# Performance work log

Measured on AMD Instinct MI355X. Metric: run time of the kernel, lower is better.

Reference implementation:

```python
import jax, jax.numpy as jnp
import numpy as np

B, RES_IN, STRIDE, RES_OUT = 8, 64, 2, 32
C_IN, C_OUT = 256, 512
H, KD, RATIO = 8, 16, 4
VD = RATIO * KD                      # 64
KV_DIM = (RATIO + 1) * KD * H        # 640
Q_DIM = KD * H                       # 128
PROJ_IN = RATIO * KD * H             # 512
SEQ = RES_IN * RES_IN                # 4096
QLEN = RES_OUT * RES_OUT             # 1024
EPS = 1e-3                           # keras BatchNormalization default epsilon


def _bn(x, gamma, beta, mean, var):
    # inference-mode batch norm over the channel axis
    return (x - mean) * (gamma * jax.lax.rsqrt(var + EPS)) + beta


def _hard_swish(x):
    return x * jnp.clip(x + 3.0, 0.0, 6.0) * (1.0 / 6.0)


def setup_inputs() -> dict:
    key = jax.random.key(0)
    ks = jax.random.split(key, 16)
    def lin(k, fan_in, fan_out):
        return jax.random.normal(k, (fan_in, fan_out), jnp.float32) / np.sqrt(fan_in)
    def bn_params(k, c):
        k1, k2, k3 = jax.random.split(k, 3)
        gamma = 1.0 + 0.1 * jax.random.normal(k1, (c,), jnp.float32)
        beta = 0.1 * jax.random.normal(k2, (c,), jnp.float32)
        mean = 0.1 * jax.random.normal(k3, (c,), jnp.float32)
        var = jax.random.uniform(jax.random.fold_in(k, 7), (c,), jnp.float32, 0.5, 1.5)
        return gamma, beta, mean, var
    x = jax.random.normal(ks[0], (B, SEQ, C_IN), jnp.float32)
    Wkv = lin(ks[1], C_IN, KV_DIM); bkv = jnp.zeros((KV_DIM,), jnp.float32)
    g_kv, b_kv, m_kv, v_kv = bn_params(ks[2], KV_DIM)
    Wq = lin(ks[3], C_IN, Q_DIM); bq = jnp.zeros((Q_DIM,), jnp.float32)
    g_q, b_q, m_q, v_q = bn_params(ks[4], Q_DIM)
    Wp = lin(ks[5], PROJ_IN, C_OUT); bp = jnp.zeros((C_OUT,), jnp.float32)
    g_p, b_p, m_p, v_p = bn_params(ks[6], C_OUT)
    return {"x": x, "Wkv": Wkv, "bkv": bkv, "g_kv": g_kv, "b_kv": b_kv, "m_kv": m_kv, "v_kv": v_kv,
            "Wq": Wq, "bq": bq, "g_q": g_q, "b_q": b_q, "m_q": m_q, "v_q": v_q,
            "Wp": Wp, "bp": bp, "g_p": g_p, "b_p": b_p, "m_p": m_p, "v_p": v_p}


def reference(x, Wkv, bkv, g_kv, b_kv, m_kv, v_kv,
              Wq, bq, g_q, b_q, m_q, v_q,
              Wp, bp, g_p, b_p, m_p, v_p):
    scale = KD ** (-0.5)
    # keys/values: Dense + BN -> [B, SEQ, H, KD+VD]
    kv = _bn(x @ Wkv + bkv, g_kv, b_kv, m_kv, v_kv)
    kv = kv.reshape(B, SEQ, H, KD + VD)
    k = jnp.transpose(kv[..., :KD], (0, 2, 1, 3))          # [B, H, SEQ, KD]
    v = jnp.transpose(kv[..., KD:], (0, 2, 1, 3))          # [B, H, SEQ, VD]
    # strided query subsample: [B, SEQ, C] -> [B, QLEN, C]
    xq = x.reshape(B, RES_IN, RES_IN, C_IN)[:, ::STRIDE, ::STRIDE].reshape(B, QLEN, C_IN)
    q = _bn(xq @ Wq + bq, g_q, b_q, m_q, v_q)
    q = jnp.transpose(q.reshape(B, QLEN, H, KD), (0, 2, 1, 3))  # [B, H, QLEN, KD]
    attn = jnp.einsum('bhqd,bhkd->bhqk', q, k) * scale
    attn = jax.nn.softmax(attn, axis=-1)                   # [B, H, QLEN, SEQ]
    av = jnp.einsum('bhqk,bhkd->bhqd', attn, v)            # [B, H, QLEN, VD]
    # faithful to TF: transpose (0,1,3,2) then reshape to (B, -1, PROJ_IN)
    out = jnp.transpose(av, (0, 1, 3, 2)).reshape(B, -1, PROJ_IN)
    out = _bn(_hard_swish(out) @ Wp + bp, g_p, b_p, m_p, v_p)
    return out
```

## Files before the change

### kernel.cpp

```cpp
#include <hip/hip_runtime.h>

typedef __bf16 bf16_t;
typedef __bf16 bf16x4 __attribute__((ext_vector_type(4)));
typedef __bf16 bf16x8 __attribute__((ext_vector_type(8)));
typedef short s16x4 __attribute__((ext_vector_type(4)));
typedef float f32x4 __attribute__((ext_vector_type(4)));

#define BN_EPS 1e-3f

#define GLOAD_LDS16(g, l) \
  __builtin_amdgcn_global_load_lds((const __attribute__((address_space(1))) void*)(g), \
                                   (__attribute__((address_space(3))) void*)(l), 16, 0, 0)

__global__ __launch_bounds__(256) void cvt_f32_bf16(
    const float* __restrict__ in, bf16_t* __restrict__ out, long n)
{
  long i = ((long)blockIdx.x * 256 + threadIdx.x) * 8;
  if (i + 8 > n) return;
  f32x4 a = *(const f32x4*)(in + i);
  f32x4 b = *(const f32x4*)(in + i + 4);
  bf16x8 o;
  o[0] = (bf16_t)a[0]; o[1] = (bf16_t)a[1]; o[2] = (bf16_t)a[2]; o[3] = (bf16_t)a[3];
  o[4] = (bf16_t)b[0]; o[5] = (bf16_t)b[1]; o[6] = (bf16_t)b[2]; o[7] = (bf16_t)b[3];
  *(bf16x8*)(out + i) = o;
}

__global__ __launch_bounds__(256) void transpose_f32_bf16(
    const float* __restrict__ in, bf16_t* __restrict__ out, int R, int C)
{
  __shared__ bf16_t t[32][33];
  int bx = blockIdx.x * 32, by = blockIdx.y * 32;
  int tx = threadIdx.x, ty = threadIdx.y;
#pragma unroll
  for (int i = 0; i < 32; i += 8)
    t[ty + i][tx] = (bf16_t)in[(long)(by + ty + i) * C + (bx + tx)];
  __syncthreads();
#pragma unroll
  for (int i = 0; i < 32; i += 8)
    out[(long)(bx + ty + i) * R + (by + tx)] = t[tx][ty + i];
}

__global__ __launch_bounds__(256) void wkv_split_transpose(
    const float* __restrict__ in, bf16_t* __restrict__ outK, bf16_t* __restrict__ outV)
{
  __shared__ bf16_t t[32][33];
  int bx = blockIdx.x * 32, by = blockIdx.y * 32;
  int tx = threadIdx.x, ty = threadIdx.y;
#pragma unroll
  for (int i = 0; i < 32; i += 8)
    t[ty + i][tx] = (bf16_t)in[(long)(by + ty + i) * 640 + (bx + tx)];
  __syncthreads();
#pragma unroll
  for (int i = 0; i < 32; i += 8) {
    int c = bx + ty + i;
    int h = c / 80, r80 = c - h * 80;
    bf16_t v = t[tx][ty + i];
    if (r80 < 16)
      outK[(long)(h * 16 + r80) * 256 + (by + tx)] = v;
    else
      outV[(long)(h * 64 + (r80 - 16)) * 256 + (by + tx)] = v;
  }
}

__global__ __launch_bounds__(512, 1) void qkv_fused(
    const bf16_t* __restrict__ xb, const bf16_t* __restrict__ Wf,
    const float* __restrict__ bkv, const float* __restrict__ g_kv,
    const float* __restrict__ b_kv, const float* __restrict__ m_kv,
    const float* __restrict__ v_kv,
    const float* __restrict__ bq, const float* __restrict__ g_q,
    const float* __restrict__ b_q, const float* __restrict__ m_q,
    const float* __restrict__ v_q,
    bf16_t* __restrict__ Kbuf, bf16_t* __restrict__ Vtb, bf16_t* __restrict__ Qbuf)
{
  __shared__ __align__(16) char Xs[65536];
  __shared__ __align__(16) char Ws[65536];

  const int tid = threadIdx.x;
  const int lane = tid & 63, w = tid >> 6;
  const int quad = lane >> 4, l15 = lane & 15;
  const int wm = w >> 2, wn = w & 3;

  const int id = blockIdx.x;
  const int xcd = id & 7, slot = id >> 3;
  const int sd6 = slot / 6;
  const int mt = xcd * 32 + sd6;
  const int nt = slot - sd6 * 6;
  const int blockM = mt * 128, blockN = nt * 128;

  {
    const int r_lo = w * 2 + (lane >> 5);
    const int soff = ((lane & 31) ^ (r_lo & 7)) << 4;
#pragma unroll
    for (int rnd = 0; rnd < 8; rnd++) {
      const int row = rnd * 16 + r_lo;
      GLOAD_LDS16((const char*)xb + (long)(blockM + row) * 512 + soff,
                  &Xs[rnd * 8192 + w * 1024]);
      GLOAD_LDS16((const char*)Wf + (long)(blockN + row) * 512 + soff,
                  &Ws[rnd * 8192 + w * 1024]);
    }
  }
  __syncthreads();

  const int sw = l15 & 7;
  f32x4 acc[4][2] = {};
#pragma unroll
  for (int ks = 0; ks < 8; ks++) {
    const int u = ks * 4 + quad;
    const int su = (u ^ sw) << 4;
    bf16x8 af[4];
#pragma unroll
    for (int mi = 0; mi < 4; mi++)
      af[mi] = *(const bf16x8*)(&Xs[(wm * 64 + mi * 16 + l15) * 512 + su]);
    bf16x8 bf_[2];
#pragma unroll
    for (int ni = 0; ni < 2; ni++)
      bf_[ni] = *(const bf16x8*)(&Ws[(wn * 32 + ni * 16 + l15) * 512 + su]);
#pragma unroll
    for (int mi = 0; mi < 4; mi++)
#pragma unroll
      for (int ni = 0; ni < 2; ni++)
        acc[mi][ni] = __builtin_amdgcn_mfma_f32_16x16x32_bf16(af[mi], bf_[ni], acc[mi][ni], 0, 0, 0);
  }

#pragma unroll
  for (int ni = 0; ni < 2; ni++) {
    const int nfbase = blockN + wn * 32 + ni * 16;
    const int col = nfbase + l15;
    float s, t, bia;
    if (nfbase < 128) {
      int cp = (col >> 4) * 80 + (col & 15);
      s = g_kv[cp] / sqrtf(v_kv[cp] + BN_EPS);
      t = b_kv[cp] - m_kv[cp] * s;
      bia = bkv[cp];
      int h = col >> 4, d = col & 15;
#pragma unroll
      for (int mi = 0; mi < 4; mi++)
#pragma unroll
        for (int r = 0; r < 4; r++) {
          int grow = blockM + wm * 64 + mi * 16 + quad * 4 + r;
          int b = grow >> 12, seq = grow & 4095;
          float y = (acc[mi][ni][r] + bia) * s + t;
          Kbuf[((long)((b * 8 + h) * 4096 + seq)) * 16 + d] = (bf16_t)y;
        }
    } else if (nfbase < 640) {
      int ch = col - 128;
      int cp = (ch >> 6) * 80 + 16 + (ch & 63);
      s = g_kv[cp] / sqrtf(v_kv[cp] + BN_EPS);
      t = b_kv[cp] - m_kv[cp] * s;
      bia = bkv[cp];
      int h2 = ch >> 6, dv = ch & 63;
#pragma unroll
      for (int mi = 0; mi < 4; mi++)
#pragma unroll
        for (int r = 0; r < 4; r++) {
          int grow = blockM + wm * 64 + mi * 16 + quad * 4 + r;
          int b = grow >> 12, seq = grow & 4095;
          int kb = seq >> 5, s32 = seq & 31;
          int qd = (s32 & 15) >> 2, j = (s32 >> 4) * 4 + (s32 & 3);
          float y = (acc[mi][ni][r] + bia) * s + t;
          Vtb[(((long)(b * 8 + h2)) << 18) + (kb << 11) + (qd << 9) + (dv << 3) + j] = (bf16_t)y;
        }
    } else {
      int qc = col - 640;
      s = g_q[qc] / sqrtf(v_q[qc] + BN_EPS);
      t = b_q[qc] - m_q[qc] * s;
      bia = bq[qc];
      int h = qc >> 4, d = qc & 15;
#pragma unroll
      for (int mi = 0; mi < 4; mi++) {
        if ((((blockM + wm * 64 + mi * 16) >> 6) & 1) != 0) continue;
#pragma unroll
        for (int r = 0; r < 4; r += 2) {
          int grow = blockM + wm * 64 + mi * 16 + quad * 4 + r;
          int b = grow >> 12, seq = grow & 4095;
          int qp = ((seq >> 7) << 5) + ((seq & 63) >> 1);
          float y = (acc[mi][ni][r] + bia) * s + t;
          Qbuf[((long)((b * 8 + h) * 1024 + qp)) * 16 + d] = (bf16_t)(y * 0.36067376f);
        }
      }
    }
  }
}

__global__ __launch_bounds__(512, 1) void proj_fused(
    const bf16_t* __restrict__ A, const bf16_t* __restrict__ Wt,
    const float* __restrict__ bias, const float* __restrict__ gamma,
    const float* __restrict__ beta, const float* __restrict__ mean,
    const float* __restrict__ var, float* __restrict__ outf)
{
  __shared__ __align__(16) char Xs[65536];
  __shared__ __align__(16) char Wl[65536];

  const int tid = threadIdx.x;
  const int lane = tid & 63, w = tid >> 6;
  const int quad = lane >> 4, l15 = lane & 15;
  const int wm = w >> 2, wn = w & 3;

  const int id = blockIdx.x;
  const int xcd = id & 7, slot = id >> 3;
  const int mt = xcd * 8 + (slot >> 2);
  const int nt = slot & 3;
  const int blockM = mt * 128, blockN = nt * 128;

  const int r_lo = w * 2 + (lane >> 5);
  const int soff = ((lane & 31) ^ (r_lo & 7)) << 4;
  const int sw = l15 & 7;
  f32x4 acc[4][2] = {};

#pragma unroll
  for (int kc = 0; kc < 2; kc++) {
    if (kc) __syncthreads();
#pragma unroll
    for (int rnd = 0; rnd < 8; rnd++) {
      const int row = rnd * 16 + r_lo;
      GLOAD_LDS16((const char*)A  + (long)(blockM + row) * 1024 + kc * 512 + soff,
                  &Xs[rnd * 8192 + w * 1024]);
      GLOAD_LDS16((const char*)Wt + (long)(blockN + row) * 1024 + kc * 512 + soff,
                  &Wl[rnd * 8192 + w * 1024]);
    }
    __syncthreads();

#pragma unroll
    for (int ks = 0; ks < 8; ks++) {
      const int u = ks * 4 + quad;
      const int su = (u ^ sw) << 4;
      bf16x8 af[4];
#pragma unroll
      for (int mi = 0; mi < 4; mi++)
        af[mi] = *(const bf16x8*)(&Xs[(wm * 64 + mi * 16 + l15) * 512 + su]);
      bf16x8 bw[2];
#pragma unroll
      for (int ni = 0; ni < 2; ni++)
        bw[ni] = *(const bf16x8*)(&Wl[(wn * 32 + ni * 16 + l15) * 512 + su]);
#pragma unroll
      for (int mi = 0; mi < 4; mi++)
#pragma unroll
        for (int ni = 0; ni < 2; ni++)
          acc[mi][ni] = __builtin_amdgcn_mfma_f32_16x16x32_bf16(af[mi], bw[ni], acc[mi][ni], 0, 0, 0);
    }
  }

#pragma unroll
  for (int ni = 0; ni < 2; ni++) {
    int col = blockN + wn * 32 + ni * 16 + l15;
    float s = gamma[col] / sqrtf(var[col] + BN_EPS);
    float t = beta[col] - mean[col] * s;
    float bia = bias[col];
#pragma unroll
    for (int mi = 0; mi < 4; mi++)
#pragma unroll
      for (int r = 0; r < 4; r++) {
        int grow = blockM + wm * 64 + mi * 16 + quad * 4 + r;
        float y = (acc[mi][ni][r] + bia) * s + t;
        outf[(long)grow * 512 + col] = y;
      }
  }
}

__global__ __launch_bounds__(256, 4) void attn_kernel(
    const bf16_t* __restrict__ Q, const bf16_t* __restrict__ K,
    const bf16_t* __restrict__ Vt, bf16_t* __restrict__ outp)
{
  const int tid = threadIdx.x;
  const int lane = tid & 63, w = tid >> 6;
  const int quad = lane >> 4, l15 = lane & 15;
  const int bh = blockIdx.x & 63, qb = blockIdx.x >> 6;
  const int b = bh >> 3, h = bh & 7;
  const bf16_t* Qp = Q + (long)bh * 1024 * 16;
  const char* Kg = (const char*)(K + (long)bh * 4096 * 16);
  const char* Vg = (const char*)(Vt + ((long)bh << 18));

  __shared__ __align__(16) char Kl[4][2048];
  __shared__ __align__(16) char Vl[4][8192];

  const int q0 = qb * 64 + w * 16;
  bf16x8 qB8;
  {
    bf16x8 qv = *(const bf16x8*)(Qp + (long)(q0 + l15) * 16 + (quad & 1) * 8);
    bf16x8 zq = {};
    qB8 = (quad < 2) ? qv : zq;
  }

  f32x4 O[4] = {};
  f32x4 lpacc = {};
  const f32x4 zf = {0.f, 0.f, 0.f, 0.f};

  bf16x8 ones8;
#pragma unroll
  for (int i = 0; i < 8; i++) ones8[i] = (bf16_t)1.f;

  const char* vsrc = Vg + (long)lane * 16;
  const char* ksrc = Kg + (long)lane * 32 + (w - 2) * 16;

  auto stage = [&](int t, int buf) {
    if (w < 2) {
#pragma unroll
      for (int c = 0; c < 2; c++)
        GLOAD_LDS16(vsrc + (long)t * 8192 + (w * 2 + c) * 1024, &Vl[buf][(w * 2 + c) * 1024]);
    } else {
#pragma unroll
      for (int c = 0; c < 2; c++)
        GLOAD_LDS16(vsrc + (long)t * 8192 + ((w - 2) * 2 + 4 + c) * 1024,
                    &Vl[buf][((w - 2) * 2 + 4 + c) * 1024]);
      GLOAD_LDS16(ksrc + (long)t * 2048, &Kl[buf][(w - 2) * 1024]);
    }
  };

  const int krow_off = (quad & 1) * 1024;

  auto compute = [&](int buf) {
#pragma unroll
    for (int kh = 0; kh < 2; kh++) {
      bf16x8 k0 = *(const bf16x8*)(&Kl[buf][krow_off + (kh * 32 + l15) * 16]);
      bf16x8 k1 = *(const bf16x8*)(&Kl[buf][krow_off + (kh * 32 + 16 + l15) * 16]);
      f32x4 S0 = __builtin_amdgcn_mfma_f32_16x16x32_bf16(k0, qB8, zf, 0, 0, 0);
      f32x4 S1 = __builtin_amdgcn_mfma_f32_16x16x32_bf16(k1, qB8, zf, 0, 0, 0);
      bf16x8 pb;
      pb[0] = (bf16_t)__builtin_amdgcn_exp2f(S0[0]);
      pb[1] = (bf16_t)__builtin_amdgcn_exp2f(S0[1]);
      pb[2] = (bf16_t)__builtin_amdgcn_exp2f(S0[2]);
      pb[3] = (bf16_t)__builtin_amdgcn_exp2f(S0[3]);
      pb[4] = (bf16_t)__builtin_amdgcn_exp2f(S1[0]);
      pb[5] = (bf16_t)__builtin_amdgcn_exp2f(S1[1]);
      pb[6] = (bf16_t)__builtin_amdgcn_exp2f(S1[2]);
      pb[7] = (bf16_t)__builtin_amdgcn_exp2f(S1[3]);
      lpacc = __builtin_amdgcn_mfma_f32_16x16x32_bf16(ones8, pb, lpacc, 0, 0, 0);
#pragma unroll
      for (int dt = 0; dt < 4; dt++) {
        bf16x8 vA = *(const bf16x8*)(&Vl[buf][kh * 4096 + quad * 1024 + (dt * 16 + l15) * 16]);
        O[dt] = __builtin_amdgcn_mfma_f32_16x16x32_bf16(vA, pb, O[dt], 0, 0, 0);
      }
    }
  };

  stage(0, 0);
  stage(1, 1);
  stage(2, 2);
#pragma unroll 4
  for (int t = 0; t < 64; t++) {
    if (t + 2 < 64) {
      if (w < 2) asm volatile("s_waitcnt vmcnt(4)" ::: "memory");
      else       asm volatile("s_waitcnt vmcnt(6)" ::: "memory");
    } else if (t + 1 < 64) {
      if (w < 2) asm volatile("s_waitcnt vmcnt(2)" ::: "memory");
      else       asm volatile("s_waitcnt vmcnt(3)" ::: "memory");
    } else {
      asm volatile("s_waitcnt vmcnt(0)" ::: "memory");
    }
    __builtin_amdgcn_s_barrier();
    __builtin_amdgcn_sched_barrier(0);
    if (t + 3 < 64) stage(t + 3, (t + 3) & 3);
    compute(t & 3);
  }

  float rl = __builtin_amdgcn_rcpf(lpacc[0]);
  int q = q0 + l15;
  long colq = q & 511;
  long rowbase = (long)b * 1024 + (long)h * 128 + (q >> 9);
#pragma unroll
  for (int dt = 0; dt < 4; dt++) {
#pragma unroll
    for (int r = 0; r < 4; r++) {
      int dv = dt * 16 + quad * 4 + r;
      float val = O[dt][r] * rl;
      float hs = val * fminf(fmaxf(val + 3.f, 0.f), 6.f) * (1.f / 6.f);
      outp[(rowbase + (long)dv * 2) * 512 + colq] = (bf16_t)hs;
    }
  }
}

extern "C" void kernel_launch(void* const* d_in, const int* in_sizes, int n_in,
                              void* d_out, int out_size, void* d_ws, size_t ws_size,
                              hipStream_t stream)
{
  const float* x    = (const float*)d_in[0];
  const float* Wkv  = (const float*)d_in[1];
  const float* bkv  = (const float*)d_in[2];
  const float* g_kv = (const float*)d_in[3];
  const float* b_kv = (const float*)d_in[4];
  const float* m_kv = (const float*)d_in[5];
  const float* v_kv = (const float*)d_in[6];
  const float* Wq   = (const float*)d_in[7];
  const float* bq   = (const float*)d_in[8];
  const float* g_q  = (const float*)d_in[9];
  const float* b_q  = (const float*)d_in[10];
  const float* m_q  = (const float*)d_in[11];
  const float* v_q  = (const float*)d_in[12];
  const float* Wp   = (const float*)d_in[13];
  const float* bp   = (const float*)d_in[14];
  const float* g_p  = (const float*)d_in[15];
  const float* b_p  = (const float*)d_in[16];
  const float* m_p  = (const float*)d_in[17];
  const float* v_p  = (const float*)d_in[18];

  char* ws = (char*)d_ws;
  bf16_t* xb   = (bf16_t*)ws; ws += (long)8 * 4096 * 256 * 2;
  bf16_t* WkT  = (bf16_t*)ws; ws += (long)128 * 256 * 2;
  bf16_t* WvT  = (bf16_t*)ws; ws += (long)512 * 256 * 2;
  bf16_t* Wq_t = (bf16_t*)ws; ws += (long)128 * 256 * 2;
  bf16_t* Wp_t = (bf16_t*)ws; ws += (long)512 * 512 * 2;
  bf16_t* Qbuf = (bf16_t*)ws; ws += (long)64 * 1024 * 16 * 2;
  bf16_t* Kbuf = (bf16_t*)ws; ws += (long)64 * 4096 * 16 * 2;
  bf16_t* Vtb  = (bf16_t*)ws; ws += (long)64 * 64 * 4096 * 2;
  bf16_t* outp = (bf16_t*)ws; ws += (long)8192 * 512 * 2;
  ws += 16384;

  cvt_f32_bf16<<<dim3(4096), 256, 0, stream>>>(x, xb, (long)8 * 4096 * 256);

  wkv_split_transpose<<<dim3(20, 8), dim3(32, 8), 0, stream>>>(Wkv, WkT, WvT);
  transpose_f32_bf16<<<dim3(4, 8),   dim3(32, 8), 0, stream>>>(Wq, Wq_t, 256, 128);
  transpose_f32_bf16<<<dim3(16, 16), dim3(32, 8), 0, stream>>>(Wp, Wp_t, 512, 512);

  qkv_fused<<<dim3(1536), 512, 0, stream>>>(xb, WkT,
      bkv, g_kv, b_kv, m_kv, v_kv, bq, g_q, b_q, m_q, v_q,
      Kbuf, Vtb, Qbuf);

  attn_kernel<<<dim3(1024), 256, 0, stream>>>(Qbuf, Kbuf, Vtb, outp);

  proj_fused<<<dim3(256), 512, 0, stream>>>(outp, Wp_t, bp, g_p, b_p, m_p, v_p, (float*)d_out);
}
```

Baseline: 213.7 us.

## Merge prep kernels and double queries per attention wave to reuse K/V tiles

The four preprocessing launches (x conversion and the three weight transposes) become one kernel that dispatches on block index, which removes launch overhead. The attention kernel now gives each wave two 16-query groups, so every K/V tile staged in LDS and every V fragment read from it serves twice as many queries. This halves the K/V global traffic and LDS reads per query. The grid is halved to 512 blocks and the launch-bounds occupancy hint drops from 4 to 2, trading fewer waves per CU for more accumulator registers.

```diff
diff --git a/kernel.cpp b/kernel.cpp
--- a/kernel.cpp
+++ b/kernel.cpp
@@ -12,53 +12,62 @@
   __builtin_amdgcn_global_load_lds((const __attribute__((address_space(1))) void*)(g), \
                                    (__attribute__((address_space(3))) void*)(l), 16, 0, 0)
 
-__global__ __launch_bounds__(256) void cvt_f32_bf16(
-    const float* __restrict__ in, bf16_t* __restrict__ out, long n)
-{
-  long i = ((long)blockIdx.x * 256 + threadIdx.x) * 8;
-  if (i + 8 > n) return;
-  f32x4 a = *(const f32x4*)(in + i);
-  f32x4 b = *(const f32x4*)(in + i + 4);
-  bf16x8 o;
-  o[0] = (bf16_t)a[0]; o[1] = (bf16_t)a[1]; o[2] = (bf16_t)a[2]; o[3] = (bf16_t)a[3];
-  o[4] = (bf16_t)b[0]; o[5] = (bf16_t)b[1]; o[6] = (bf16_t)b[2]; o[7] = (bf16_t)b[3];
-  *(bf16x8*)(out + i) = o;
-}
-
-__global__ __launch_bounds__(256) void transpose_f32_bf16(
-    const float* __restrict__ in, bf16_t* __restrict__ out, int R, int C)
+__global__ __launch_bounds__(256) void prep(
+    const float* __restrict__ x, bf16_t* __restrict__ xb,
+    const float* __restrict__ Wkv, bf16_t* __restrict__ outK, bf16_t* __restrict__ outV,
+    const float* __restrict__ Wq, bf16_t* __restrict__ Wq_t,
+    const float* __restrict__ Wp, bf16_t* __restrict__ Wp_t)
 {
   __shared__ bf16_t t[32][33];
-  int bx = blockIdx.x * 32, by = blockIdx.y * 32;
-  int tx = threadIdx.x, ty = threadIdx.y;
-#pragma unroll
-  for (int i = 0; i < 32; i += 8)
-    t[ty + i][tx] = (bf16_t)in[(long)(by + ty + i) * C + (bx + tx)];
-  __syncthreads();
-#pragma unroll
-  for (int i = 0; i < 32; i += 8)
-    out[(long)(bx + ty + i) * R + (by + tx)] = t[tx][ty + i];
-}
-
-__global__ __launch_bounds__(256) void wkv_split_transpose(
-    const float* __restrict__ in, bf16_t* __restrict__ outK, bf16_t* __restrict__ outV)
-{
-  __shared__ bf16_t t[32][33];
-  int bx = blockIdx.x * 32, by = blockIdx.y * 32;
-  int tx = threadIdx.x, ty = threadIdx.y;
-#pragma unroll
-  for (int i = 0; i < 32; i += 8)
-    t[ty + i][tx] = (bf16_t)in[(long)(by + ty + i) * 640 + (bx + tx)];
-  __syncthreads();
-#pragma unroll
-  for (int i = 0; i < 32; i += 8) {
-    int c = bx + ty + i;
-    int h = c / 80, r80 = c - h * 80;
-    bf16_t v = t[tx][ty + i];
-    if (r80 < 16)
-      outK[(long)(h * 16 + r80) * 256 + (by + tx)] = v;
-    else
-      outV[(long)(h * 64 + (r80 - 16)) * 256 + (by + tx)] = v;
+  const int id = blockIdx.x;
+  if (id < 4096) {
+    long i = ((long)id * 256 + threadIdx.x) * 8;
+    f32x4 a = *(const f32x4*)(x + i);
+    f32x4 b = *(const f32x4*)(x + i + 4);
+    bf16x8 o;
+    o[0] = (bf16_t)a[0]; o[1] = (bf16_t)a[1]; o[2] = (bf16_t)a[2]; o[3] = (bf16_t)a[3];
+    o[4] = (bf16_t)b[0]; o[5] = (bf16_t)b[1]; o[6] = (bf16_t)b[2]; o[7] = (bf16_t)b[3];
+    *(bf16x8*)(xb + i) = o;
+    return;
+  }
+  const int tx = threadIdx.x & 31, ty = threadIdx.x >> 5;
+  if (id < 4256) {
+    int id2 = id - 4096;
+    int bx = (id2 % 20) * 32, by = (id2 / 20) * 32;
+#pragma unroll
+    for (int i = 0; i < 32; i += 8)
+      t[ty + i][tx] = (bf16_t)Wkv[(long)(by + ty + i) * 640 + (bx + tx)];
+    __syncthreads();
+#pragma unroll
+    for (int i = 0; i < 32; i += 8) {
+      int c = bx + ty + i;
+      int h = c / 80, r80 = c - h * 80;
+      bf16_t v = t[tx][ty + i];
+      if (r80 < 16)
+        outK[(long)(h * 16 + r80) * 256 + (by + tx)] = v;
+      else
+        outV[(long)(h * 64 + (r80 - 16)) * 256 + (by + tx)] = v;
+    }
+  } else if (id < 4288) {
+    int id3 = id - 4256;
+    int bx = (id3 & 3) * 32, by = (id3 >> 2) * 32;
+#pragma unroll
+    for (int i = 0; i < 32; i += 8)
+      t[ty + i][tx] = (bf16_t)Wq[(long)(by + ty + i) * 128 + (bx + tx)];
+    __syncthreads();
+#pragma unroll
+    for (int i = 0; i < 32; i += 8)
+      Wq_t[(long)(bx + ty + i) * 256 + (by + tx)] = t[tx][ty + i];
+  } else {
+    int id4 = id - 4288;
+    int bx = (id4 & 15) * 32, by = (id4 >> 4) * 32;
+#pragma unroll
+    for (int i = 0; i < 32; i += 8)
+      t[ty + i][tx] = (bf16_t)Wp[(long)(by + ty + i) * 512 + (bx + tx)];
+    __syncthreads();
+#pragma unroll
+    for (int i = 0; i < 32; i += 8)
+      Wp_t[(long)(bx + ty + i) * 512 + (by + tx)] = t[tx][ty + i];
   }
 }
 
@@ -257,7 +266,7 @@
   }
 }
 
-__global__ __launch_bounds__(256, 4) void attn_kernel(
+__global__ __launch_bounds__(256, 2) void attn_kernel(
     const bf16_t* __restrict__ Q, const bf16_t* __restrict__ K,
     const bf16_t* __restrict__ Vt, bf16_t* __restrict__ outp)
 {
@@ -273,16 +282,17 @@
   __shared__ __align__(16) char Kl[4][2048];
   __shared__ __align__(16) char Vl[4][8192];
 
-  const int q0 = qb * 64 + w * 16;
-  bf16x8 qB8;
-  {
-    bf16x8 qv = *(const bf16x8*)(Qp + (long)(q0 + l15) * 16 + (quad & 1) * 8);
+  const int q0 = qb * 128 + w * 32;
+  bf16x8 qB8[2];
+#pragma unroll
+  for (int g = 0; g < 2; g++) {
+    bf16x8 qv = *(const bf16x8*)(Qp + (long)(q0 + g * 16 + l15) * 16 + (quad & 1) * 8);
     bf16x8 zq = {};
-    qB8 = (quad < 2) ? qv : zq;
-  }
-
-  f32x4 O[4] = {};
-  f32x4 lpacc = {};
+    qB8[g] = (quad < 2) ? qv : zq;
+  }
+
+  f32x4 O[2][4] = {};
+  f32x4 lpacc[2] = {};
   const f32x4 zf = {0.f, 0.f, 0.f, 0.f};
 
   bf16x8 ones8;
@@ -313,22 +323,27 @@
     for (int kh = 0; kh < 2; kh++) {
       bf16x8 k0 = *(const bf16x8*)(&Kl[buf][krow_off + (kh * 32 + l15) * 16]);
       bf16x8 k1 = *(const bf16x8*)(&Kl[buf][krow_off + (kh * 32 + 16 + l15) * 16]);
-      f32x4 S0 = __builtin_amdgcn_mfma_f32_16x16x32_bf16(k0, qB8, zf, 0, 0, 0);
-      f32x4 S1 = __builtin_amdgcn_mfma_f32_16x16x32_bf16(k1, qB8, zf, 0, 0, 0);
-      bf16x8 pb;
-      pb[0] = (bf16_t)__builtin_amdgcn_exp2f(S0[0]);
-      pb[1] = (bf16_t)__builtin_amdgcn_exp2f(S0[1]);
-      pb[2] = (bf16_t)__builtin_amdgcn_exp2f(S0[2]);
-      pb[3] = (bf16_t)__builtin_amdgcn_exp2f(S0[3]);
-      pb[4] = (bf16_t)__builtin_amdgcn_exp2f(S1[0]);
-      pb[5] = (bf16_t)__builtin_amdgcn_exp2f(S1[1]);
-      pb[6] = (bf16_t)__builtin_amdgcn_exp2f(S1[2]);
-      pb[7] = (bf16_t)__builtin_amdgcn_exp2f(S1[3]);
-      lpacc = __builtin_amdgcn_mfma_f32_16x16x32_bf16(ones8, pb, lpacc, 0, 0, 0);
-#pragma unroll
-      for (int dt = 0; dt < 4; dt++) {
-        bf16x8 vA = *(const bf16x8*)(&Vl[buf][kh * 4096 + quad * 1024 + (dt * 16 + l15) * 16]);
-        O[dt] = __builtin_amdgcn_mfma_f32_16x16x32_bf16(vA, pb, O[dt], 0, 0, 0);
+      bf16x8 vA[4];
+#pragma unroll
+      for (int dt = 0; dt < 4; dt++)
+        vA[dt] = *(const bf16x8*)(&Vl[buf][kh * 4096 + quad * 1024 + (dt * 16 + l15) * 16]);
+#pragma unroll
+      for (int g = 0; g < 2; g++) {
+        f32x4 S0 = __builtin_amdgcn_mfma_f32_16x16x32_bf16(k0, qB8[g], zf, 0, 0, 0);
+        f32x4 S1 = __builtin_amdgcn_mfma_f32_16x16x32_bf16(k1, qB8[g], zf, 0, 0, 0);
+        bf16x8 pb;
+        pb[0] = (bf16_t)__builtin_amdgcn_exp2f(S0[0]);
+        pb[1] = (bf16_t)__builtin_amdgcn_exp2f(S0[1]);
+        pb[2] = (bf16_t)__builtin_amdgcn_exp2f(S0[2]);
+        pb[3] = (bf16_t)__builtin_amdgcn_exp2f(S0[3]);
+        pb[4] = (bf16_t)__builtin_amdgcn_exp2f(S1[0]);
+        pb[5] = (bf16_t)__builtin_amdgcn_exp2f(S1[1]);
+        pb[6] = (bf16_t)__builtin_amdgcn_exp2f(S1[2]);
+        pb[7] = (bf16_t)__builtin_amdgcn_exp2f(S1[3]);
+        lpacc[g] = __builtin_amdgcn_mfma_f32_16x16x32_bf16(ones8, pb, lpacc[g], 0, 0, 0);
+#pragma unroll
+        for (int dt = 0; dt < 4; dt++)
+          O[g][dt] = __builtin_amdgcn_mfma_f32_16x16x32_bf16(vA[dt], pb, O[g][dt], 0, 0, 0);
       }
     }
   };
@@ -353,18 +368,21 @@
     compute(t & 3);
   }
 
-  float rl = __builtin_amdgcn_rcpf(lpacc[0]);
-  int q = q0 + l15;
-  long colq = q & 511;
-  long rowbase = (long)b * 1024 + (long)h * 128 + (q >> 9);
-#pragma unroll
-  for (int dt = 0; dt < 4; dt++) {
-#pragma unroll
-    for (int r = 0; r < 4; r++) {
-      int dv = dt * 16 + quad * 4 + r;
-      float val = O[dt][r] * rl;
-      float hs = val * fminf(fmaxf(val + 3.f, 0.f), 6.f) * (1.f / 6.f);
-      outp[(rowbase + (long)dv * 2) * 512 + colq] = (bf16_t)hs;
+#pragma unroll
+  for (int g = 0; g < 2; g++) {
+    float rl = __builtin_amdgcn_rcpf(lpacc[g][0]);
+    int q = q0 + g * 16 + l15;
+    long colq = q & 511;
+    long rowbase = (long)b * 1024 + (long)h * 128 + (q >> 9);
+#pragma unroll
+    for (int dt = 0; dt < 4; dt++) {
+#pragma unroll
+      for (int r = 0; r < 4; r++) {
+        int dv = dt * 16 + quad * 4 + r;
+        float val = O[g][dt][r] * rl;
+        float hs = val * fminf(fmaxf(val + 3.f, 0.f), 6.f) * (1.f / 6.f);
+        outp[(rowbase + (long)dv * 2) * 512 + colq] = (bf16_t)hs;
+      }
     }
   }
 }
@@ -405,17 +423,13 @@
   bf16_t* outp = (bf16_t*)ws; ws += (long)8192 * 512 * 2;
   ws += 16384;
 
-  cvt_f32_bf16<<<dim3(4096), 256, 0, stream>>>(x, xb, (long)8 * 4096 * 256);
-
-  wkv_split_transpose<<<dim3(20, 8), dim3(32, 8), 0, stream>>>(Wkv, WkT, WvT);
-  transpose_f32_bf16<<<dim3(4, 8),   dim3(32, 8), 0, stream>>>(Wq, Wq_t, 256, 128);
-  transpose_f32_bf16<<<dim3(16, 16), dim3(32, 8), 0, stream>>>(Wp, Wp_t, 512, 512);
+  prep<<<dim3(4544), 256, 0, stream>>>(x, xb, Wkv, WkT, WvT, Wq, Wq_t, Wp, Wp_t);
 
   qkv_fused<<<dim3(1536), 512, 0, stream>>>(xb, WkT,
       bkv, g_kv, b_kv, m_kv, v_kv, bq, g_q, b_q, m_q, v_q,
       Kbuf, Vtb, Qbuf);
 
-  attn_kernel<<<dim3(1024), 256, 0, stream>>>(Qbuf, Kbuf, Vtb, outp);
+  attn_kernel<<<dim3(512), 256, 0, stream>>>(Qbuf, Kbuf, Vtb, outp);
 
   proj_fused<<<dim3(256), 512, 0, stream>>>(outp, Wp_t, bp, g_p, b_p, m_p, v_p, (float*)d_out);
 }
```

After: 208.9 us. 1.02x faster.
